# Optimization experiments

Measured on AMD Instinct MI355X. Metric: run time of the kernel, lower is better.

Reference implementation:

```python
import math
import jax, jax.numpy as jnp
import numpy as np


def _unskew(X):
    # X: B x M x (M+L)  ->  B x M x L (each row i shifted left by i)
    B, M, MpL = X.shape
    L = MpL - M
    X = X.reshape(B, M * MpL)
    X = jnp.pad(X, ((0, 0), (0, M)))          # B x (M*(M+L)+M)
    X = X.reshape(B, M, MpL + 1)               # B x M x (M+L+1)
    return X[:, :, :L]


def _skew(X, pad_value):
    # X: B x M x L  ->  B x M x (M+L) (each row i shifted right by i)
    B, M, L = X.shape
    X = jnp.pad(X, ((0, 0), (0, 0), (0, M + 1)), constant_values=pad_value)
    X = X.reshape(B, -1)[:, :-M]               # B x (M*(M+L))
    return X.reshape(B, M, M + L)


def setup_inputs() -> dict:
    key = jax.random.key(0)
    k1, k2, k3, k4 = jax.random.split(key, 4)
    B, M, L, H = 128, 512, 1024, 64   # B = batch*heads, key len = M+L
    query = jax.random.normal(k1, (B, M, H), dtype=jnp.float32)
    key_t = jax.random.normal(k2, (B, M + L, H), dtype=jnp.float32)
    value = jax.random.normal(k3, (B, M + L, H), dtype=jnp.float32)
    key_pe = jax.random.normal(k4, (1, H, L), dtype=jnp.float32) * 0.02
    return {"query": query, "key": key_t, "value": value, "key_pe": key_pe}


def reference(query, key, value, key_pe):
    H = query.shape[-1]  # head_dim
    # content attention: B x M x (M+L), then unskew to relative coords B x M x L
    attn_cont = jnp.einsum('bmh,bnh->bmn', query, key)
    attn_cont = _unskew(attn_cont)
    # position attention: B x M x L (key_pe broadcasts over batch)
    attn_pos = jnp.einsum('bmh,xhl->bml', query, key_pe)
    attn = (attn_cont + attn_pos) / math.sqrt(H)
    attn = jax.nn.softmax(attn, axis=-1)
    # dropout p=0.0 -> identity
    attn_sk = _skew(attn, 0.0)                  # B x M x (M+L)
    out = jnp.einsum('bmn,bnh->bmh', attn_sk, value)
    return out
```

## Files before the change

kernel.cpp:

```cpp
#include <hip/hip_runtime.h>
#include <math.h>

typedef __bf16 bf16x8 __attribute__((ext_vector_type(8)));
typedef __bf16 bf16x4 __attribute__((ext_vector_type(4)));
typedef float  f32x4  __attribute__((ext_vector_type(4)));
typedef short  s16x4  __attribute__((ext_vector_type(4)));

constexpr int B_  = 128;
constexpr int M_  = 512;
constexpr int L_  = 1024;
constexpr int H_  = 64;
constexpr int KL_ = 1536;

constexpr int BM  = 64;
constexpr int KT  = 64;
constexpr int NT  = 17;
constexpr int PPC = 192;

constexpr int OFF_VT   = 0;
constexpr int OFF_PPOS = 16384;
constexpr int SMEM_BYTES = 40960;
constexpr int OFF_OBUF = 0;
constexpr int OFF_LSUM = 18432;
constexpr int OBS = 36;

constexpr size_t PET_BYTES = 16 * 2 * 2 * 64 * 16 * sizeof(__bf16);

#define MFMA32(A, B, C) __builtin_amdgcn_mfma_f32_16x16x32_bf16((A), (B), (C), 0, 0, 0)

static __device__ __forceinline__ f32x4 mfma_pv(bf16x4 a, bf16x4 b, f32x4 c) {
  return __builtin_amdgcn_mfma_f32_16x16x16bf16_1k(
      __builtin_bit_cast(s16x4, a), __builtin_bit_cast(s16x4, b), c, 0, 0, 0);
}

constexpr float EXP2_SCALE = 0.18033688011112042f;

static __device__ __forceinline__ int vt_idx(int hrow, int kv) {
  return hrow * 64 + (kv ^ ((hrow & 15) << 2));
}
static __device__ __forceinline__ int pp_idx(int row, int col) {
  return row * PPC + (col ^ ((row & 15) << 2));
}

__global__ void pe_pack(const float* __restrict__ PE, __bf16* __restrict__ PET) {
  const int gid = blockIdx.x * 256 + threadIdx.x;
  const int j   = gid & 7;
  const int f   = (gid >> 3) & 1;
  const int ln  = (gid >> 4) & 63;
  const int blk = gid >> 10;
  const int c   = blk & 1;
  const int nt  = (blk >> 1) & 1;
  const int ch  = blk >> 2;
  const int nid = ln & 15, qid = ln >> 4;
  const int h = 8 * qid + j + 32 * f;
  const int l = 64 * ch + 32 * c + 16 * nt + nid;
  PET[gid] = (__bf16)PE[h * L_ + l];
}

template <bool USE_PET>
__global__ __launch_bounds__(256, 2)
void seqattn_v11(const float* __restrict__ Q, const float* __restrict__ K,
                 const float* __restrict__ V, const float* __restrict__ PE,
                 const __bf16* __restrict__ PET, float* __restrict__ O) {
  __shared__ alignas(16) char smem[SMEM_BYTES];
  __bf16* vtb  = (__bf16*)(smem + OFF_VT);
  __bf16* ppos = (__bf16*)(smem + OFF_PPOS);

  const int tid  = threadIdx.x;
  const int w    = tid >> 6;
  const int lane = tid & 63;
  const int nid  = lane & 15;
  const int qid  = lane >> 4;
  const int a    = w >> 1;
  const int c    = w & 1;
  const int b    = blockIdx.x;
  const int m0   = blockIdx.y * BM;

  const int vj = (tid & 15) * 4, vh = (tid >> 4) * 4;

  const float* peg = &PE[(size_t)(8 * qid) * L_ + 32 * c + nid];

  bf16x8 aq[2][2];
  #pragma unroll
  for (int it = 0; it < 2; ++it) {
    const float* qg = &Q[((size_t)b * M_ + m0 + 32 * a + 16 * it + nid) * H_];
    #pragma unroll
    for (int j = 0; j < 8; ++j) {
      aq[it][0][j] = (__bf16)qg[8 * qid + j];
      aq[it][1][j] = (__bf16)qg[32 + 8 * qid + j];
    }
  }

  f32x4 o[2][4];
  float lpart[2] = {0.f, 0.f};
  #pragma unroll
  for (int it = 0; it < 2; ++it)
    #pragma unroll
    for (int ht = 0; ht < 4; ++ht) o[it][ht] = (f32x4){0.f, 0.f, 0.f, 0.f};

  bf16x8 ak[2][2];
  #pragma unroll
  for (int nt = 0; nt < 2; ++nt) {
    const float* kg = &K[((size_t)b * KL_ + m0 + 32 * c + 16 * nt + nid) * H_ + 8 * qid];
    const f32x4 k0 = *(const f32x4*)kg;
    const f32x4 k1 = *(const f32x4*)(kg + 4);
    const f32x4 k2 = *(const f32x4*)(kg + 32);
    const f32x4 k3 = *(const f32x4*)(kg + 36);
    #pragma unroll
    for (int j = 0; j < 4; ++j) {
      ak[nt][0][j] = (__bf16)k0[j]; ak[nt][0][4 + j] = (__bf16)k1[j];
      ak[nt][1][j] = (__bf16)k2[j]; ak[nt][1][4 + j] = (__bf16)k3[j];
    }
  }
  f32x4 vr[4];
  {
    const float* vg = &V[((size_t)b * KL_ + m0 + vj) * H_ + vh];
    #pragma unroll
    for (int e = 0; e < 4; ++e) vr[e] = *(const f32x4*)(vg + e * H_);
  }
  {
    const f32x4 z = {0.f, 0.f, 0.f, 0.f};
    bf16x8 pf0[2], pf1[2];
    if constexpr (USE_PET) {
      const __bf16* pb = PET + (size_t)c * 1024 + (size_t)lane * 16;
      pf0[0] = *(const bf16x8*)pb;          pf1[0] = *(const bf16x8*)(pb + 8);
      pf0[1] = *(const bf16x8*)(pb + 2048); pf1[1] = *(const bf16x8*)(pb + 2048 + 8);
    } else {
      #pragma unroll
      for (int nt = 0; nt < 2; ++nt)
        #pragma unroll
        for (int j = 0; j < 8; ++j) {
          pf0[nt][j] = (__bf16)peg[(size_t)j * L_ + 16 * nt];
          pf1[nt][j] = (__bf16)peg[(size_t)(32 + j) * L_ + 16 * nt];
        }
    }
    #pragma unroll
    for (int nt = 0; nt < 2; ++nt) {
      #pragma unroll
      for (int it = 0; it < 2; ++it) {
        f32x4 pp = MFMA32(pf0[nt], aq[it][0], z);
        pp = MFMA32(pf1[nt], aq[it][1], pp);
        const int row = 32 * a + 16 * it + nid;
        const int cb  = 32 * c + 16 * nt + 4 * qid + row;
        #pragma unroll
        for (int r = 0; r < 4; ++r)
          ppos[pp_idx(row, (cb + r) % PPC)] = (__bf16)pp[r];
      }
    }
  }
  #pragma unroll
  for (int e = 0; e < 4; ++e) {
    bf16x4 y = {(__bf16)vr[0][e], (__bf16)vr[1][e], (__bf16)vr[2][e], (__bf16)vr[3][e]};
    *(bf16x4*)&vtb[vt_idx(vh + e, vj)] = y;
  }
  __syncthreads();

  for (int t = 0; t < NT; ++t) {
    bf16x4 pe4[2][2];
    #pragma unroll
    for (int it = 0; it < 2; ++it) {
      const int row = 32 * a + 16 * it + nid;
      #pragma unroll
      for (int nt = 0; nt < 2; ++nt)
        pe4[it][nt] = *(const bf16x4*)
            &ppos[pp_idx(row, 64 * (t % 3) + 32 * c + 16 * nt + 4 * qid)];
    }

    bf16x8 pf0[2], pf1[2];
    if (t < 15) {
      if constexpr (USE_PET) {
        const __bf16* pb = PET + ((size_t)(t + 1) * 4 + c) * 1024 + (size_t)lane * 16;
        pf0[0] = *(const bf16x8*)pb;          pf1[0] = *(const bf16x8*)(pb + 8);
        pf0[1] = *(const bf16x8*)(pb + 2048); pf1[1] = *(const bf16x8*)(pb + 2048 + 8);
      } else {
        const float* pc = peg + (t + 1) * 64;
        #pragma unroll
        for (int nt = 0; nt < 2; ++nt)
          #pragma unroll
          for (int j = 0; j < 8; ++j) {
            pf0[nt][j] = (__bf16)pc[(size_t)j * L_ + 16 * nt];
            pf1[nt][j] = (__bf16)pc[(size_t)(32 + j) * L_ + 16 * nt];
          }
      }
    }

    if (t < 16) {
      const float* vg = &V[((size_t)b * KL_ + m0 + KT * (t + 1) + vj) * H_ + vh];
      #pragma unroll
      for (int e = 0; e < 4; ++e) vr[e] = *(const f32x4*)(vg + e * H_);
    }

    const __bf16* vtt = vtb + (t & 1) * 64 * 64;
    const f32x4 z = {0.f, 0.f, 0.f, 0.f};

    f32x4 s[2][2];
    #pragma unroll
    for (int nt = 0; nt < 2; ++nt)
      #pragma unroll
      for (int it = 0; it < 2; ++it) {
        s[it][nt] = MFMA32(ak[nt][0], aq[it][0], z);
        s[it][nt] = MFMA32(ak[nt][1], aq[it][1], s[it][nt]);
      }

    if (t < 16) {
      const int j1 = m0 + KT * (t + 1);
      #pragma unroll
      for (int nt = 0; nt < 2; ++nt) {
        const float* kg = &K[((size_t)b * KL_ + j1 + 32 * c + 16 * nt + nid) * H_ + 8 * qid];
        const f32x4 k0 = *(const f32x4*)kg;
        const f32x4 k1 = *(const f32x4*)(kg + 4);
        const f32x4 k2 = *(const f32x4*)(kg + 32);
        const f32x4 k3 = *(const f32x4*)(kg + 36);
        #pragma unroll
        for (int j = 0; j < 4; ++j) {
          ak[nt][0][j] = (__bf16)k0[j]; ak[nt][0][4 + j] = (__bf16)k1[j];
          ak[nt][1][j] = (__bf16)k2[j]; ak[nt][1][4 + j] = (__bf16)k3[j];
        }
      }
    }

    if (t < 15) {
      const int chb = 64 * (t + 1);
      #pragma unroll
      for (int nt = 0; nt < 2; ++nt) {
        #pragma unroll
        for (int it = 0; it < 2; ++it) {
          f32x4 pp = MFMA32(pf0[nt], aq[it][0], z);
          pp = MFMA32(pf1[nt], aq[it][1], pp);
          const int row = 32 * a + 16 * it + nid;
          const int cb  = chb + 32 * c + 16 * nt + 4 * qid + row;
          #pragma unroll
          for (int r = 0; r < 4; ++r)
            ppos[pp_idx(row, (cb + r) % PPC)] = (__bf16)pp[r];
        }
      }
    }

    const bool edge = (t == 0) || (t == 16);
    bf16x4 pa[2][2];
    #pragma unroll
    for (int it = 0; it < 2; ++it) {
      const int row = 32 * a + 16 * it + nid;
      #pragma unroll
      for (int nt = 0; nt < 2; ++nt) {
        const int lb = KT * t + 32 * c + 16 * nt + 4 * qid - row;
        #pragma unroll
        for (int r = 0; r < 4; ++r) {
          const int l = lb + r;
          float p;
          if (!edge || (unsigned)l < 1024u)
            p = exp2f((s[it][nt][r] + (float)pe4[it][nt][r]) * EXP2_SCALE);
          else
            p = 0.f;
          lpart[it] += p;
          pa[it][nt][r] = (__bf16)p;
        }
      }
    }

    #pragma unroll
    for (int nt = 0; nt < 2; ++nt) {
      bf16x4 vb[4];
      #pragma unroll
      for (int ht = 0; ht < 4; ++ht)
        vb[ht] = *(const bf16x4*)&vtt[vt_idx(16 * ht + nid, 32 * c + 16 * nt + 4 * qid)];
      #pragma unroll
      for (int it = 0; it < 2; ++it)
        #pragma unroll
        for (int ht = 0; ht < 4; ++ht)
          o[it][ht] = mfma_pv(pa[it][nt], vb[ht], o[it][ht]);
    }

    if (t < 16) {
      __bf16* vtn = vtb + ((t + 1) & 1) * 64 * 64;
      #pragma unroll
      for (int e = 0; e < 4; ++e) {
        bf16x4 y = {(__bf16)vr[0][e], (__bf16)vr[1][e], (__bf16)vr[2][e], (__bf16)vr[3][e]};
        *(bf16x4*)&vtn[vt_idx(vh + e, vj)] = y;
      }
    }
    __syncthreads();
  }

  float* lsum = (float*)(smem + OFF_LSUM);
  float* obuf = (float*)(smem + OFF_OBUF);

  #pragma unroll
  for (int it = 0; it < 2; ++it) {
    float v = lpart[it];
    v += __shfl_xor(v, 16);
    v += __shfl_xor(v, 32);
    lpart[it] = v;
  }
  if (qid == 0) {
    #pragma unroll
    for (int it = 0; it < 2; ++it)
      lsum[c * 64 + 32 * a + 16 * it + nid] = lpart[it];
  }
  if (c == 1) {
    #pragma unroll
    for (int it = 0; it < 2; ++it)
      #pragma unroll
      for (int ht = 0; ht < 4; ++ht)
        *(f32x4*)&obuf[(a * 64 + 16 * ht + nid) * OBS + 16 * it + 4 * qid] = o[it][ht];
  }
  __syncthreads();
  if (c == 0) {
    float inv[2][4];
    #pragma unroll
    for (int it = 0; it < 2; ++it)
      #pragma unroll
      for (int r = 0; r < 4; ++r) {
        const int row = 32 * a + 16 * it + 4 * qid + r;
        inv[it][r] = 1.f / (lsum[row] + lsum[64 + row]);
      }
    #pragma unroll
    for (int it = 0; it < 2; ++it) {
      #pragma unroll
      for (int ht = 0; ht < 4; ++ht) {
        f32x4 oo = o[it][ht] +
                   *(const f32x4*)&obuf[(a * 64 + 16 * ht + nid) * OBS + 16 * it + 4 * qid];
        #pragma unroll
        for (int r = 0; r < 4; ++r) {
          const int row = 32 * a + 16 * it + 4 * qid + r;
          O[((size_t)b * M_ + m0 + row) * H_ + 16 * ht + nid] = oo[r] * inv[it][r];
        }
      }
    }
  }
}

extern "C" void kernel_launch(void* const* d_in, const int* in_sizes, int n_in,
                              void* d_out, int out_size, void* d_ws, size_t ws_size,
                              hipStream_t stream) {
  const float* Q  = (const float*)d_in[0];
  const float* K  = (const float*)d_in[1];
  const float* V  = (const float*)d_in[2];
  const float* PE = (const float*)d_in[3];
  float* O = (float*)d_out;

  dim3 grid(B_, M_ / BM);
  if (d_ws != nullptr && ws_size >= PET_BYTES) {
    __bf16* PET = (__bf16*)d_ws;
    hipLaunchKernelGGL(pe_pack, dim3(256), dim3(256), 0, stream, PE, PET);
    hipLaunchKernelGGL(seqattn_v11<true>, grid, dim3(256), 0, stream, Q, K, V, PE, PET, O);
  } else {
    hipLaunchKernelGGL(seqattn_v11<false>, grid, dim3(256), 0, stream, Q, K, V, PE,
                       (const __bf16*)nullptr, O);
  }
}
```

Baseline: 226.2 us.

## Stage probabilities in LDS and split PV output columns across warps

Each warp now writes its bf16 softmax probabilities to a shared P tile. The PV matmul is then repartitioned so each warp computes all 64 key columns for half of the head dimension. This removes the end-of-kernel cross-warp output reduction through shared memory and halves the per-warp output accumulators. In exchange it adds a second __syncthreads per tile, drops V double-buffering (V is written at the top of each iteration), and adds LDS traffic for P.

```diff
diff --git a/kernel.cpp b/kernel.cpp
--- a/kernel.cpp
+++ b/kernel.cpp
@@ -18,11 +18,10 @@
 constexpr int PPC = 192;
 
 constexpr int OFF_VT   = 0;
+constexpr int OFF_P    = 8192;
 constexpr int OFF_PPOS = 16384;
 constexpr int SMEM_BYTES = 40960;
-constexpr int OFF_OBUF = 0;
-constexpr int OFF_LSUM = 18432;
-constexpr int OBS = 36;
+constexpr int OFF_LSUM = 16384;
 
 constexpr size_t PET_BYTES = 16 * 2 * 2 * 64 * 16 * sizeof(__bf16);
 
@@ -35,8 +34,8 @@
 
 constexpr float EXP2_SCALE = 0.18033688011112042f;
 
-static __device__ __forceinline__ int vt_idx(int hrow, int kv) {
-  return hrow * 64 + (kv ^ ((hrow & 15) << 2));
+static __device__ __forceinline__ int sw_idx(int row, int col) {
+  return row * 64 + (col ^ ((row & 15) << 2));
 }
 static __device__ __forceinline__ int pp_idx(int row, int col) {
   return row * PPC + (col ^ ((row & 15) << 2));
@@ -59,11 +58,12 @@
 
 template <bool USE_PET>
 __global__ __launch_bounds__(256, 2)
-void seqattn_v11(const float* __restrict__ Q, const float* __restrict__ K,
+void seqattn_v12(const float* __restrict__ Q, const float* __restrict__ K,
                  const float* __restrict__ V, const float* __restrict__ PE,
                  const __bf16* __restrict__ PET, float* __restrict__ O) {
   __shared__ alignas(16) char smem[SMEM_BYTES];
   __bf16* vtb  = (__bf16*)(smem + OFF_VT);
+  __bf16* Pl   = (__bf16*)(smem + OFF_P);
   __bf16* ppos = (__bf16*)(smem + OFF_PPOS);
 
   const int tid  = threadIdx.x;
@@ -91,12 +91,12 @@
     }
   }
 
-  f32x4 o[2][4];
+  f32x4 o[2][2];
   float lpart[2] = {0.f, 0.f};
   #pragma unroll
   for (int it = 0; it < 2; ++it)
     #pragma unroll
-    for (int ht = 0; ht < 4; ++ht) o[it][ht] = (f32x4){0.f, 0.f, 0.f, 0.f};
+    for (int ht = 0; ht < 2; ++ht) o[it][ht] = (f32x4){0.f, 0.f, 0.f, 0.f};
 
   bf16x8 ak[2][2];
   #pragma unroll
@@ -148,24 +148,69 @@
       }
     }
   }
-  #pragma unroll
-  for (int e = 0; e < 4; ++e) {
-    bf16x4 y = {(__bf16)vr[0][e], (__bf16)vr[1][e], (__bf16)vr[2][e], (__bf16)vr[3][e]};
-    *(bf16x4*)&vtb[vt_idx(vh + e, vj)] = y;
-  }
   __syncthreads();
 
   for (int t = 0; t < NT; ++t) {
-    bf16x4 pe4[2][2];
-    #pragma unroll
-    for (int it = 0; it < 2; ++it) {
-      const int row = 32 * a + 16 * it + nid;
-      #pragma unroll
-      for (int nt = 0; nt < 2; ++nt)
-        pe4[it][nt] = *(const bf16x4*)
+    #pragma unroll
+    for (int e = 0; e < 4; ++e) {
+      bf16x4 y = {(__bf16)vr[0][e], (__bf16)vr[1][e], (__bf16)vr[2][e], (__bf16)vr[3][e]};
+      *(bf16x4*)&vtb[sw_idx(vh + e, vj)] = y;
+    }
+    if (t < 16) {
+      const float* vg = &V[((size_t)b * KL_ + m0 + KT * (t + 1) + vj) * H_ + vh];
+      #pragma unroll
+      for (int e = 0; e < 4; ++e) vr[e] = *(const f32x4*)(vg + e * H_);
+    }
+
+    const f32x4 z = {0.f, 0.f, 0.f, 0.f};
+    const bool edge = (t == 0) || (t == 16);
+
+    #pragma unroll
+    for (int nt = 0; nt < 2; ++nt) {
+      f32x4 s0 = MFMA32(ak[nt][0], aq[0][0], z);
+      s0 = MFMA32(ak[nt][1], aq[0][1], s0);
+      f32x4 s1 = MFMA32(ak[nt][0], aq[1][0], z);
+      s1 = MFMA32(ak[nt][1], aq[1][1], s1);
+      #pragma unroll
+      for (int it = 0; it < 2; ++it) {
+        const f32x4 sv = it ? s1 : s0;
+        const int row = 32 * a + 16 * it + nid;
+        const bf16x4 pe4 = *(const bf16x4*)
             &ppos[pp_idx(row, 64 * (t % 3) + 32 * c + 16 * nt + 4 * qid)];
-    }
-
+        const int lb = KT * t + 32 * c + 16 * nt + 4 * qid - row;
+        bf16x4 pav;
+        #pragma unroll
+        for (int r = 0; r < 4; ++r) {
+          const int l = lb + r;
+          float p;
+          if (!edge || (unsigned)l < 1024u)
+            p = exp2f((sv[r] + (float)pe4[r]) * EXP2_SCALE);
+          else
+            p = 0.f;
+          lpart[it] += p;
+          pav[r] = (__bf16)p;
+        }
+        *(bf16x4*)&Pl[sw_idx(row, 32 * c + 16 * nt + 4 * qid)] = pav;
+      }
+    }
+    __syncthreads();
+
+    if (t < 16) {
+      const int j1 = m0 + KT * (t + 1);
+      #pragma unroll
+      for (int nt = 0; nt < 2; ++nt) {
+        const float* kg = &K[((size_t)b * KL_ + j1 + 32 * c + 16 * nt + nid) * H_ + 8 * qid];
+        const f32x4 k0 = *(const f32x4*)kg;
+        const f32x4 k1 = *(const f32x4*)(kg + 4);
+        const f32x4 k2 = *(const f32x4*)(kg + 32);
+        const f32x4 k3 = *(const f32x4*)(kg + 36);
+        #pragma unroll
+        for (int j = 0; j < 4; ++j) {
+          ak[nt][0][j] = (__bf16)k0[j]; ak[nt][0][4 + j] = (__bf16)k1[j];
+          ak[nt][1][j] = (__bf16)k2[j]; ak[nt][1][4 + j] = (__bf16)k3[j];
+        }
+      }
+    }
     bf16x8 pf0[2], pf1[2];
     if (t < 15) {
       if constexpr (USE_PET) {
@@ -184,39 +229,17 @@
       }
     }
 
-    if (t < 16) {
-      const float* vg = &V[((size_t)b * KL_ + m0 + KT * (t + 1) + vj) * H_ + vh];
-      #pragma unroll
-      for (int e = 0; e < 4; ++e) vr[e] = *(const f32x4*)(vg + e * H_);
-    }
-
-    const __bf16* vtt = vtb + (t & 1) * 64 * 64;
-    const f32x4 z = {0.f, 0.f, 0.f, 0.f};
-
-    f32x4 s[2][2];
-    #pragma unroll
-    for (int nt = 0; nt < 2; ++nt)
-      #pragma unroll
-      for (int it = 0; it < 2; ++it) {
-        s[it][nt] = MFMA32(ak[nt][0], aq[it][0], z);
-        s[it][nt] = MFMA32(ak[nt][1], aq[it][1], s[it][nt]);
-      }
-
-    if (t < 16) {
-      const int j1 = m0 + KT * (t + 1);
-      #pragma unroll
-      for (int nt = 0; nt < 2; ++nt) {
-        const float* kg = &K[((size_t)b * KL_ + j1 + 32 * c + 16 * nt + nid) * H_ + 8 * qid];
-        const f32x4 k0 = *(const f32x4*)kg;
-        const f32x4 k1 = *(const f32x4*)(kg + 4);
-        const f32x4 k2 = *(const f32x4*)(kg + 32);
-        const f32x4 k3 = *(const f32x4*)(kg + 36);
-        #pragma unroll
-        for (int j = 0; j < 4; ++j) {
-          ak[nt][0][j] = (__bf16)k0[j]; ak[nt][0][4 + j] = (__bf16)k1[j];
-          ak[nt][1][j] = (__bf16)k2[j]; ak[nt][1][4 + j] = (__bf16)k3[j];
-        }
-      }
+    #pragma unroll
+    for (int ks = 0; ks < 4; ++ks) {
+      const int kv = 16 * ks + 4 * qid;
+      const bf16x4 pa0 = *(const bf16x4*)&Pl[sw_idx(32 * a + nid, kv)];
+      const bf16x4 pa1 = *(const bf16x4*)&Pl[sw_idx(32 * a + 16 + nid, kv)];
+      const bf16x4 vb0 = *(const bf16x4*)&vtb[sw_idx(32 * c + nid, kv)];
+      const bf16x4 vb1 = *(const bf16x4*)&vtb[sw_idx(32 * c + 16 + nid, kv)];
+      o[0][0] = mfma_pv(pa0, vb0, o[0][0]);
+      o[0][1] = mfma_pv(pa0, vb1, o[0][1]);
+      o[1][0] = mfma_pv(pa1, vb0, o[1][0]);
+      o[1][1] = mfma_pv(pa1, vb1, o[1][1]);
     }
 
     if (t < 15) {
@@ -235,55 +258,10 @@
         }
       }
     }
-
-    const bool edge = (t == 0) || (t == 16);
-    bf16x4 pa[2][2];
-    #pragma unroll
-    for (int it = 0; it < 2; ++it) {
-      const int row = 32 * a + 16 * it + nid;
-      #pragma unroll
-      for (int nt = 0; nt < 2; ++nt) {
-        const int lb = KT * t + 32 * c + 16 * nt + 4 * qid - row;
-        #pragma unroll
-        for (int r = 0; r < 4; ++r) {
-          const int l = lb + r;
-          float p;
-          if (!edge || (unsigned)l < 1024u)
-            p = exp2f((s[it][nt][r] + (float)pe4[it][nt][r]) * EXP2_SCALE);
-          else
-            p = 0.f;
-          lpart[it] += p;
-          pa[it][nt][r] = (__bf16)p;
-        }
-      }
-    }
-
-    #pragma unroll
-    for (int nt = 0; nt < 2; ++nt) {
-      bf16x4 vb[4];
-      #pragma unroll
-      for (int ht = 0; ht < 4; ++ht)
-        vb[ht] = *(const bf16x4*)&vtt[vt_idx(16 * ht + nid, 32 * c + 16 * nt + 4 * qid)];
-      #pragma unroll
-      for (int it = 0; it < 2; ++it)
-        #pragma unroll
-        for (int ht = 0; ht < 4; ++ht)
-          o[it][ht] = mfma_pv(pa[it][nt], vb[ht], o[it][ht]);
-    }
-
-    if (t < 16) {
-      __bf16* vtn = vtb + ((t + 1) & 1) * 64 * 64;
-      #pragma unroll
-      for (int e = 0; e < 4; ++e) {
-        bf16x4 y = {(__bf16)vr[0][e], (__bf16)vr[1][e], (__bf16)vr[2][e], (__bf16)vr[3][e]};
-        *(bf16x4*)&vtn[vt_idx(vh + e, vj)] = y;
-      }
-    }
     __syncthreads();
   }
 
   float* lsum = (float*)(smem + OFF_LSUM);
-  float* obuf = (float*)(smem + OFF_OBUF);
 
   #pragma unroll
   for (int it = 0; it < 2; ++it) {
@@ -297,34 +275,25 @@
     for (int it = 0; it < 2; ++it)
       lsum[c * 64 + 32 * a + 16 * it + nid] = lpart[it];
   }
-  if (c == 1) {
-    #pragma unroll
-    for (int it = 0; it < 2; ++it)
-      #pragma unroll
-      for (int ht = 0; ht < 4; ++ht)
-        *(f32x4*)&obuf[(a * 64 + 16 * ht + nid) * OBS + 16 * it + 4 * qid] = o[it][ht];
-  }
   __syncthreads();
-  if (c == 0) {
-    float inv[2][4];
-    #pragma unroll
-    for (int it = 0; it < 2; ++it)
+
+  float inv[2][4];
+  #pragma unroll
+  for (int it = 0; it < 2; ++it)
+    #pragma unroll
+    for (int r = 0; r < 4; ++r) {
+      const int row = 32 * a + 16 * it + 4 * qid + r;
+      inv[it][r] = 1.f / (lsum[row] + lsum[64 + row]);
+    }
+  #pragma unroll
+  for (int it = 0; it < 2; ++it) {
+    #pragma unroll
+    for (int ht = 0; ht < 2; ++ht) {
       #pragma unroll
       for (int r = 0; r < 4; ++r) {
         const int row = 32 * a + 16 * it + 4 * qid + r;
-        inv[it][r] = 1.f / (lsum[row] + lsum[64 + row]);
-      }
-    #pragma unroll
-    for (int it = 0; it < 2; ++it) {
-      #pragma unroll
-      for (int ht = 0; ht < 4; ++ht) {
-        f32x4 oo = o[it][ht] +
-                   *(const f32x4*)&obuf[(a * 64 + 16 * ht + nid) * OBS + 16 * it + 4 * qid];
-        #pragma unroll
-        for (int r = 0; r < 4; ++r) {
-          const int row = 32 * a + 16 * it + 4 * qid + r;
-          O[((size_t)b * M_ + m0 + row) * H_ + 16 * ht + nid] = oo[r] * inv[it][r];
-        }
+        O[((size_t)b * M_ + m0 + row) * H_ + 32 * c + 16 * ht + nid] =
+            o[it][ht][r] * inv[it][r];
       }
     }
   }
@@ -343,9 +312,9 @@
   if (d_ws != nullptr && ws_size >= PET_BYTES) {
     __bf16* PET = (__bf16*)d_ws;
     hipLaunchKernelGGL(pe_pack, dim3(256), dim3(256), 0, stream, PE, PET);
-    hipLaunchKernelGGL(seqattn_v11<true>, grid, dim3(256), 0, stream, Q, K, V, PE, PET, O);
+    hipLaunchKernelGGL(seqattn_v12<true>, grid, dim3(256), 0, stream, Q, K, V, PE, PET, O);
   } else {
-    hipLaunchKernelGGL(seqattn_v11<false>, grid, dim3(256), 0, stream, Q, K, V, PE,
+    hipLaunchKernelGGL(seqattn_v12<false>, grid, dim3(256), 0, stream, Q, K, V, PE,
                        (const __bf16*)nullptr, O);
   }
 }
```

After: 224.7 us. No clear change (-0.6%).
